# Optimization experiments

Measured on AMD Instinct MI355X. Metric: run time of the kernel, lower is better.

Reference implementation:

```python
import jax, jax.numpy as jnp
import numpy as np

EMBED_DIM = 1024
NUM_HEADS = 16
HEAD_DIM = EMBED_DIM // NUM_HEADS


def setup_inputs() -> dict:
    key = jax.random.key(0)
    ks = jax.random.split(key, 12)
    B, Nq, Nkv, D = 4, 1024, 1024, EMBED_DIM
    s = 1.0 / np.sqrt(D)
    return {
        "query": jax.random.normal(ks[0], (B, Nq, D), jnp.float32),
        "key_value": jax.random.normal(ks[1], (B, Nkv, D), jnp.float32),
        "Wq": jax.random.normal(ks[2], (D, D), jnp.float32) * s,
        "bq": jnp.zeros((D,), jnp.float32),
        "Wk": jax.random.normal(ks[3], (D, D), jnp.float32) * s,
        "bk": jnp.zeros((D,), jnp.float32),
        "Wv": jax.random.normal(ks[4], (D, D), jnp.float32) * s,
        "bv": jnp.zeros((D,), jnp.float32),
        "Wo": jax.random.normal(ks[5], (D, D), jnp.float32) * s,
        "bo": jnp.zeros((D,), jnp.float32),
        "gamma": jnp.ones((D,), jnp.float32),
        "beta": jnp.zeros((D,), jnp.float32),
    }


def reference(query, key_value, Wq, bq, Wk, bk, Wv, bv, Wo, bo, gamma, beta):
    B, Nq, D = query.shape
    Nkv = key_value.shape[1]
    H, Hd = NUM_HEADS, HEAD_DIM
    # projections -> [B, H, N, Hd]
    q = (query @ Wq + bq).reshape(B, Nq, H, Hd).transpose(0, 2, 1, 3)
    k = (key_value @ Wk + bk).reshape(B, Nkv, H, Hd).transpose(0, 2, 1, 3)
    v = (key_value @ Wv + bv).reshape(B, Nkv, H, Hd).transpose(0, 2, 1, 3)
    scores = jnp.einsum("bhqd,bhkd->bhqk", q, k) / jnp.sqrt(jnp.float32(Hd))
    attn = jax.nn.softmax(scores, axis=-1)  # dropout = identity at eval
    out = jnp.einsum("bhqk,bhkd->bhqd", attn, v)
    out = out.transpose(0, 2, 1, 3).reshape(B, Nq, D)
    out = out @ Wo + bo
    # residual + LayerNorm (eps = 1e-5, torch default)
    x = query + out
    mu = jnp.mean(x, axis=-1, keepdims=True)
    var = jnp.mean(jnp.square(x - mu), axis=-1, keepdims=True)
    return (x - mu) / jnp.sqrt(var + 1e-5) * gamma + beta
```

## Files before the change

### kernel.cpp

```cpp
#include <hip/hip_runtime.h>

typedef unsigned short u16;
typedef unsigned int u32;
typedef __attribute__((ext_vector_type(4))) unsigned short u16x4;
typedef __attribute__((ext_vector_type(8))) short short8;
typedef __attribute__((ext_vector_type(4))) float f32x4;

#define MFMA16(a, b, c) __builtin_amdgcn_mfma_f32_16x16x32_bf16(a, b, c, 0, 0, 0)

__device__ __forceinline__ u16 f2bf(float f) {
  unsigned u = __builtin_bit_cast(unsigned, f);
  u += 0x7fffu + ((u >> 16) & 1u);
  return (u16)(u >> 16);
}

__device__ __forceinline__ u32 cvtpk(float lo, float hi) {
  u32 r;
  asm("v_cvt_pk_bf16_f32 %0, %1, %2" : "=v"(r) : "v"(lo), "v"(hi));
  return r;
}

__device__ __forceinline__ float ex2(float x) {
  float r;
  asm("v_exp_f32 %0, %1" : "=v"(r) : "v"(x));
  return r;
}

__device__ __forceinline__ void gl_lds16(const void* g, void* l) {
  __builtin_amdgcn_global_load_lds((const __attribute__((address_space(1))) char*)g,
                                   (__attribute__((address_space(3))) char*)l, 16, 0, 0);
}

__global__ __launch_bounds__(256) void cvt_bf16_k(const float* __restrict__ in,
                                                  u16* __restrict__ out) {
  int i = blockIdx.x * 256 + threadIdx.x;
  float4 v = ((const float4*)in)[i];
  u16x4 o;
  o.x = f2bf(v.x); o.y = f2bf(v.y); o.z = f2bf(v.z); o.w = f2bf(v.w);
  ((u16x4*)out)[i] = o;
}

__global__ __launch_bounds__(256) void wt_k(const float* __restrict__ W0, const float* __restrict__ W1,
                                            const float* __restrict__ W2, const float* __restrict__ W3,
                                            u16* __restrict__ T0, u16* __restrict__ T1,
                                            u16* __restrict__ T2, u16* __restrict__ T3) {
  const float* W; u16* T;
  switch (blockIdx.z) {
    case 0: W = W0; T = T0; break;
    case 1: W = W1; T = T1; break;
    case 2: W = W2; T = T2; break;
    default: W = W3; T = T3; break;
  }
  __shared__ __align__(16) u16 t[64][72];
  const int k0 = blockIdx.y * 64, n0 = blockIdx.x * 64;
  const int tid = threadIdx.x;
  const int r = tid >> 4, c4 = (tid & 15) * 4;
#pragma unroll
  for (int i = 0; i < 4; i++) {
    float4 v = *(const float4*)(W + (k0 + r + i * 16) * 1024 + n0 + c4);
    u16x4 o;
    o.x = f2bf(v.x); o.y = f2bf(v.y); o.z = f2bf(v.z); o.w = f2bf(v.w);
    *(u16x4*)&t[r + i * 16][c4] = o;
  }
  __syncthreads();
#pragma unroll
  for (int i = 0; i < 4; i++) {
    int nr = r + i * 16;
    u16x4 o;
    o.x = t[c4 + 0][nr]; o.y = t[c4 + 1][nr]; o.z = t[c4 + 2][nr]; o.w = t[c4 + 3][nr];
    *(u16x4*)(T + (n0 + nr) * 1024 + k0 + c4) = o;
  }
}

__global__ __launch_bounds__(256, 3) void gemmqkv_k(
    const u16* __restrict__ qbf, const u16* __restrict__ kvbf,
    const u16* __restrict__ Wqt, const u16* __restrict__ Wkt, const u16* __restrict__ Wvt,
    const float* __restrict__ pbq, const float* __restrict__ pbk, const float* __restrict__ pbv,
    u16* __restrict__ Qh, u16* __restrict__ Kh, u16* __restrict__ Vth) {
  const int lin = blockIdx.x;
  const int swz = (lin & 7) * 96 + (lin >> 3);
  const int x = swz & 7, y = (swz >> 3) & 31, z = swz >> 8;

  const u16* A  = (z == 0) ? qbf : kvbf;
  const u16* Bt = (z == 0) ? Wqt : (z == 1 ? Wkt : Wvt);
  const float* bias = (z == 0) ? pbq : (z == 1 ? pbk : pbv);

  __shared__ __align__(16) u16 As[128 * 64];
  __shared__ __align__(16) u16 Bs[128 * 64];
  const int tid = threadIdx.x;
  const int l = tid & 63, w = tid >> 6;
  const int lr = l >> 4, lc = l & 15;
  const int wr = w >> 1, wc = w & 1;
  const int m0 = y * 128, n0 = x * 128;

  f32x4 acc[4][4] = {};

  const int sr = tid >> 2, sc = (tid & 3) * 8;
  const u16* Ag = A + (m0 + sr) * 1024 + sc;
  const u16* Bg = Bt + (n0 + sr) * 1024 + sc;

  for (int k0 = 0; k0 < 1024; k0 += 64) {
    __syncthreads();
    gl_lds16(Ag + k0, As + tid * 8);
    gl_lds16(Ag + 64 * 1024 + k0, As + 2048 + tid * 8);
    gl_lds16(Bg + k0, Bs + tid * 8);
    gl_lds16(Bg + 64 * 1024 + k0, Bs + 2048 + tid * 8);
    gl_lds16(Ag + k0 + 32, As + 4096 + tid * 8);
    gl_lds16(Ag + 64 * 1024 + k0 + 32, As + 6144 + tid * 8);
    gl_lds16(Bg + k0 + 32, Bs + 4096 + tid * 8);
    gl_lds16(Bg + 64 * 1024 + k0 + 32, Bs + 6144 + tid * 8);
    __syncthreads();
    const u16* PA = (z == 2) ? Bs : As;
    const u16* PB = (z == 2) ? As : Bs;
    short8 af[4][2], bf[4][2];
    const int ks8 = lr * 8;
#pragma unroll
    for (int m = 0; m < 4; m++)
#pragma unroll
      for (int h = 0; h < 2; h++)
        af[m][h] = *(const short8*)(PA + h * 4096 + (wr * 64 + m * 16 + lc) * 32 + ks8);
#pragma unroll
    for (int n = 0; n < 4; n++)
#pragma unroll
      for (int h = 0; h < 2; h++)
        bf[n][h] = *(const short8*)(PB + h * 4096 + (wc * 64 + n * 16 + lc) * 32 + ks8);
#pragma unroll
    for (int m = 0; m < 4; m++)
#pragma unroll
      for (int n = 0; n < 4; n++) {
        acc[m][n] = MFMA16(af[m][0], bf[n][0], acc[m][n]);
        acc[m][n] = MFMA16(af[m][1], bf[n][1], acc[m][n]);
      }
  }

  if (z == 2) {
#pragma unroll
    for (int m = 0; m < 4; m++) {
#pragma unroll
      for (int r = 0; r < 4; r++) {
        int ncol = n0 + wr * 64 + m * 16 + lr * 4 + r;
        float bb = bias[ncol];
        int h = ncol >> 6, d = ncol & 63;
#pragma unroll
        for (int n = 0; n < 4; n++) {
          int tok = m0 + wc * 64 + n * 16 + lc;
          Vth[(((tok >> 10) * 16 + h) * 64 + d) * 1024 + (tok & 1023)] =
              f2bf(acc[m][n][r] + bb);
        }
      }
    }
  } else {
    u16* outb = (z == 0) ? Qh : Kh;
    const float scale = (z == 0) ? 0.18033688f : 1.0f;
#pragma unroll
    for (int m = 0; m < 4; m++)
#pragma unroll
      for (int n = 0; n < 4; n++) {
        int ncol = n0 + wc * 64 + n * 16 + lc;
        float bb = bias[ncol];
        int h = ncol >> 6, d = ncol & 63;
#pragma unroll
        for (int r = 0; r < 4; r++) {
          int tok = m0 + wr * 64 + m * 16 + lr * 4 + r;
          outb[(((tok >> 10) * 16 + h) * 1024 + (tok & 1023)) * 64 + d] =
              f2bf((acc[m][n][r] + bb) * scale);
        }
      }
  }
}

__global__ __launch_bounds__(256, 4) void gemmo_k(const u16* __restrict__ A,
                                                  const u16* __restrict__ Bt,
                                                  const float* __restrict__ bias,
                                                  float* __restrict__ outf) {
  const int lin = blockIdx.x;
  const int swz = (lin & 7) * 64 + (lin >> 3);
  const int x = swz & 15, y = swz >> 4;

  __shared__ __align__(16) u16 As[128 * 32];
  __shared__ __align__(16) u16 Bs[64 * 32];
  const int tid = threadIdx.x;
  const int l = tid & 63, w = tid >> 6;
  const int lr = l >> 4, lc = l & 15;
  const int wr = w >> 1, wc = w & 1;
  const int m0 = y * 128, n0 = x * 64;

  f32x4 acc[4][2] = {};
  const int sc = (tid & 3) * 8;
  const u16* Ag = A + (m0 + (tid >> 2)) * 1024 + sc;
  const u16* Bg = Bt + (n0 + (tid >> 2)) * 1024 + sc;

  for (int k0 = 0; k0 < 1024; k0 += 32) {
    __syncthreads();
    gl_lds16(Ag + k0, As + tid * 8);
    gl_lds16(Ag + 64 * 1024 + k0, As + 2048 + tid * 8);
    gl_lds16(Bg + k0, Bs + tid * 8);
    __syncthreads();
    short8 af[4], bf[2];
    const int ks8 = lr * 8;
#pragma unroll
    for (int m = 0; m < 4; m++)
      af[m] = *(const short8*)(As + (wr * 64 + m * 16 + lc) * 32 + ks8);
#pragma unroll
    for (int n = 0; n < 2; n++)
      bf[n] = *(const short8*)(Bs + (wc * 32 + n * 16 + lc) * 32 + ks8);
#pragma unroll
    for (int m = 0; m < 4; m++)
#pragma unroll
      for (int n = 0; n < 2; n++)
        acc[m][n] = MFMA16(af[m], bf[n], acc[m][n]);
  }
#pragma unroll
  for (int m = 0; m < 4; m++)
#pragma unroll
    for (int n = 0; n < 2; n++) {
      int ncol = n0 + wc * 32 + n * 16 + lc;
      float bb = bias[ncol];
#pragma unroll
      for (int r = 0; r < 4; r++) {
        int tok = m0 + wr * 64 + m * 16 + lr * 4 + r;
        outf[tok * 1024 + ncol] = acc[m][n][r] + bb;
      }
    }
}

__global__ __launch_bounds__(256, 4) void attn_k(const u16* __restrict__ Q,
                                                 const u16* __restrict__ K,
                                                 const u16* __restrict__ Vt,
                                                 u16* __restrict__ O) {
  const int bid = blockIdx.x;
  const int xcd = bid & 7, j = bid >> 3;
  const int bh = xcd + 8 * (j & 7);
  const int q0 = (j >> 3) * 64;
  const int tid = threadIdx.x;
  const int w = tid >> 6, l = tid & 63;
  const int lr = l >> 4, lc = l & 15;
  const u16* Qh = Q + bh * (1024 * 64);
  const u16* Kh = K + bh * (1024 * 64);
  const u16* Vh = Vt + bh * (64 * 1024);

  __shared__ __align__(16) u16 Ks[2][64 * 64];
  __shared__ __align__(16) u16 Vs[2][64 * 64];
  __shared__ __align__(16) u32 Plds[4][16][32];

  const int st_row = tid >> 3;
  const int st_cb = (tid & 7) * 16;
  const int sw1 = (st_cb ^ ((st_row & 7) << 4)) >> 1;
  const int st_row2 = st_row + 32;
  const int sw2 = (st_cb ^ ((st_row2 & 7) << 4)) >> 1;

  short8 bq[2];
#pragma unroll
  for (int ks = 0; ks < 2; ks++)
    bq[ks] = *(const short8*)(Qh + (q0 + w * 16 + lc) * 64 + ks * 32 + lr * 8);

  f32x4 oacc[4] = {};
  float mrun = -1e30f, lrun = 0.f;

  gl_lds16(Kh + st_row * 64 + sw1, &Ks[0][tid * 8]);
  gl_lds16(Kh + st_row2 * 64 + sw2, &Ks[0][2048 + tid * 8]);
  gl_lds16(Vh + st_row * 1024 + sw1, &Vs[0][tid * 8]);
  gl_lds16(Vh + st_row2 * 1024 + sw2, &Vs[0][2048 + tid * 8]);

  const int xw = (lc & 7) << 2;

  for (int t = 0; t < 16; ++t) {
    const int pb = t & 1;
    if (t < 15) {
      const int kvn = (t + 1) * 64;
      gl_lds16(Kh + (kvn + st_row) * 64 + sw1, &Ks[pb ^ 1][tid * 8]);
      gl_lds16(Kh + (kvn + st_row2) * 64 + sw2, &Ks[pb ^ 1][2048 + tid * 8]);
      gl_lds16(Vh + st_row * 1024 + kvn + sw1, &Vs[pb ^ 1][tid * 8]);
      gl_lds16(Vh + st_row2 * 1024 + kvn + sw2, &Vs[pb ^ 1][2048 + tid * 8]);
      asm volatile("s_waitcnt vmcnt(4)" ::: "memory");
    } else {
      asm volatile("s_waitcnt vmcnt(0)" ::: "memory");
    }
    __builtin_amdgcn_s_barrier();
    asm volatile("" ::: "memory");

    const u16* Kb = Ks[pb];
    const u16* Vb = Vs[pb];

    f32x4 s[4] = {};
    __builtin_amdgcn_s_setprio(1);
#pragma unroll
    for (int mk = 0; mk < 4; mk++) {
      const int krow = mk * 16 + lc;
      const u16* kp = Kb + krow * 64;
#pragma unroll
      for (int ks = 0; ks < 2; ks++) {
        const int cb = (ks * 64 + lr * 16) ^ ((krow & 7) << 4);
        short8 ak = *(const short8*)(kp + (cb >> 1));
        s[mk] = MFMA16(ak, bq[ks], s[mk]);
      }
    }
    __builtin_amdgcn_s_setprio(0);

    float mx;
    {
      float a = fmaxf(fmaxf(s[0][0], s[0][1]), fmaxf(s[0][2], s[0][3]));
      float b = fmaxf(fmaxf(s[1][0], s[1][1]), fmaxf(s[1][2], s[1][3]));
      float c = fmaxf(fmaxf(s[2][0], s[2][1]), fmaxf(s[2][2], s[2][3]));
      float d = fmaxf(fmaxf(s[3][0], s[3][1]), fmaxf(s[3][2], s[3][3]));
      mx = fmaxf(fmaxf(a, b), fmaxf(c, d));
    }
    mx = fmaxf(mx, __shfl_xor(mx, 16));
    mx = fmaxf(mx, __shfl_xor(mx, 32));

    if (!__all(mx <= mrun + 8.f)) {
      float mnew = fmaxf(mrun, mx);
      float alpha = ex2(mrun - mnew);
      mrun = mnew;
      lrun *= alpha;
      float alr[4];
#pragma unroll
      for (int r = 0; r < 4; r++) alr[r] = __shfl(alpha, lr * 4 + r);
#pragma unroll
      for (int nd = 0; nd < 4; nd++)
#pragma unroll
        for (int r = 0; r < 4; r++) oacc[nd][r] *= alr[r];
    }

#pragma unroll
    for (int mk = 0; mk < 4; mk++)
#pragma unroll
      for (int r = 0; r < 4; r++) s[mk][r] = ex2(s[mk][r] - mrun);
    float ps;
    {
      float a = (s[0][0] + s[0][1]) + (s[0][2] + s[0][3]);
      float b = (s[1][0] + s[1][1]) + (s[1][2] + s[1][3]);
      float c = (s[2][0] + s[2][1]) + (s[2][2] + s[2][3]);
      float d = (s[3][0] + s[3][1]) + (s[3][2] + s[3][3]);
      ps = (a + b) + (c + d);
    }
    ps += __shfl_xor(ps, 16);
    ps += __shfl_xor(ps, 32);
    lrun += ps;

    u32* PW = &Plds[w][lc][0];
#pragma unroll
    for (int mk = 0; mk < 4; mk++)
#pragma unroll
      for (int rr = 0; rr < 2; rr++)
        PW[(mk * 8 + lr * 2 + rr) ^ xw] = cvtpk(s[mk][2 * rr], s[mk][2 * rr + 1]);

    __builtin_amdgcn_s_setprio(1);
#pragma unroll
    for (int ks = 0; ks < 2; ks++) {
      short8 ap = *(const short8*)&Plds[w][lc][(ks * 16 + lr * 4) ^ xw];
#pragma unroll
      for (int nd = 0; nd < 4; nd++) {
        const int vrow = nd * 16 + lc;
        const int cb = (ks * 64 + lr * 16) ^ ((vrow & 7) << 4);
        short8 bv = *(const short8*)(Vb + vrow * 64 + (cb >> 1));
        oacc[nd] = MFMA16(ap, bv, oacc[nd]);
      }
    }
    __builtin_amdgcn_s_setprio(0);

    asm volatile("" ::: "memory");
    __builtin_amdgcn_s_barrier();
  }

  float inv = 1.f / lrun;
  float invr[4];
#pragma unroll
  for (int r = 0; r < 4; r++) invr[r] = __shfl(inv, lr * 4 + r);
  const int b = bh >> 4, h = bh & 15;
#pragma unroll
  for (int r = 0; r < 4; r++) {
    int row = b * 1024 + q0 + w * 16 + lr * 4 + r;
#pragma unroll
    for (int nd = 0; nd < 4; nd++)
      O[row * 1024 + h * 64 + nd * 16 + lc] = f2bf(oacc[nd][r] * invr[r]);
  }
}

__global__ __launch_bounds__(256) void ln_k(const float* __restrict__ q,
                                            const float* __restrict__ p2,
                                            const float* __restrict__ gamma,
                                            const float* __restrict__ beta,
                                            float* __restrict__ out) {
  const int row = blockIdx.x, tid = threadIdx.x;
  float4 xq = ((const float4*)(q + row * 1024))[tid];
  float4 xp = ((const float4*)(p2 + row * 1024))[tid];
  float4 x = {xq.x + xp.x, xq.y + xp.y, xq.z + xp.z, xq.w + xp.w};
  float s = x.x + x.y + x.z + x.w;
#pragma unroll
  for (int off = 1; off < 64; off <<= 1) s += __shfl_xor(s, off);
  __shared__ float red[8];
  const int w = tid >> 6;
  if ((tid & 63) == 0) red[w] = s;
  __syncthreads();
  float mu = (red[0] + red[1] + red[2] + red[3]) * (1.0f / 1024.0f);
  float4 dx = {x.x - mu, x.y - mu, x.z - mu, x.w - mu};
  float s2 = dx.x * dx.x + dx.y * dx.y + dx.z * dx.z + dx.w * dx.w;
#pragma unroll
  for (int off = 1; off < 64; off <<= 1) s2 += __shfl_xor(s2, off);
  if ((tid & 63) == 0) red[4 + w] = s2;
  __syncthreads();
  float var = (red[4] + red[5] + red[6] + red[7]) * (1.0f / 1024.0f);
  float rs = rsqrtf(var + 1e-5f);
  float4 g = ((const float4*)gamma)[tid];
  float4 bb = ((const float4*)beta)[tid];
  float4 o = {dx.x * rs * g.x + bb.x, dx.y * rs * g.y + bb.y,
              dx.z * rs * g.z + bb.z, dx.w * rs * g.w + bb.w};
  ((float4*)(out + row * 1024))[tid] = o;
}

extern "C" void kernel_launch(void* const* d_in, const int* in_sizes, int n_in,
                              void* d_out, int out_size, void* d_ws, size_t ws_size,
                              hipStream_t stream) {
  const float* query = (const float*)d_in[0];
  const float* kv    = (const float*)d_in[1];
  const float* Wq = (const float*)d_in[2];
  const float* bq = (const float*)d_in[3];
  const float* Wk = (const float*)d_in[4];
  const float* bk = (const float*)d_in[5];
  const float* Wv = (const float*)d_in[6];
  const float* bv = (const float*)d_in[7];
  const float* Wo = (const float*)d_in[8];
  const float* bo = (const float*)d_in[9];
  const float* gamma = (const float*)d_in[10];
  const float* beta  = (const float*)d_in[11];
  float* out = (float*)d_out;

  char* ws = (char*)d_ws;
  const size_t MB = 1u << 20;
  u16* qbf  = (u16*)(ws + 0 * MB);
  u16* kvbf = (u16*)(ws + 8 * MB);
  u16* Wqt  = (u16*)(ws + 16 * MB);
  u16* Wkt  = (u16*)(ws + 18 * MB);
  u16* Wvt  = (u16*)(ws + 20 * MB);
  u16* Wot  = (u16*)(ws + 22 * MB);
  u16* Qh   = (u16*)(ws + 24 * MB);
  u16* Kh   = (u16*)(ws + 32 * MB);
  u16* Vth  = (u16*)(ws + 40 * MB);
  u16* attO = (u16*)(ws + 48 * MB);
  float* p2 = (float*)(ws + 56 * MB);

  cvt_bf16_k<<<dim3(4096), dim3(256), 0, stream>>>(query, qbf);
  cvt_bf16_k<<<dim3(4096), dim3(256), 0, stream>>>(kv, kvbf);
  wt_k<<<dim3(16, 16, 4), dim3(256), 0, stream>>>(Wq, Wk, Wv, Wo, Wqt, Wkt, Wvt, Wot);

  gemmqkv_k<<<dim3(768), dim3(256), 0, stream>>>(qbf, kvbf, Wqt, Wkt, Wvt,
                                                 bq, bk, bv, Qh, Kh, Vth);

  attn_k<<<dim3(1024), dim3(256), 0, stream>>>(Qh, Kh, Vth, attO);

  gemmo_k<<<dim3(512), dim3(256), 0, stream>>>(attO, Wot, bo, p2);

  ln_k<<<dim3(4096), dim3(256), 0, stream>>>(query, p2, gamma, beta, out);
}
```

Measured before the change: 113.0 us.

## Double query rows per attention block and merge bf16 conversion launches

Each attention block now covers 128 query rows instead of 64. Every wave handles two 16-row groups that share each K/V tile loaded into LDS, which halves the grid and halves K/V global-to-LDS traffic per query. The two fp32-to-bf16 conversion kernels are also merged into a single launch to save one launch. The cost is more registers per thread, with launch bounds dropped to 2 blocks per SIMD, and fewer blocks to keep the device busy.

```diff
diff --git a/kernel.cpp b/kernel.cpp
--- a/kernel.cpp
+++ b/kernel.cpp
@@ -31,9 +31,13 @@
                                    (__attribute__((address_space(3))) char*)l, 16, 0, 0);
 }
 
-__global__ __launch_bounds__(256) void cvt_bf16_k(const float* __restrict__ in,
-                                                  u16* __restrict__ out) {
-  int i = blockIdx.x * 256 + threadIdx.x;
+__global__ __launch_bounds__(256) void cvt2_k(const float* __restrict__ a,
+                                              const float* __restrict__ b,
+                                              u16* __restrict__ oa, u16* __restrict__ ob) {
+  const int bid = blockIdx.x;
+  const float* in = (bid < 4096) ? a : b;
+  u16* out = (bid < 4096) ? oa : ob;
+  int i = (bid & 4095) * 256 + threadIdx.x;
   float4 v = ((const float4*)in)[i];
   u16x4 o;
   o.x = f2bf(v.x); o.y = f2bf(v.y); o.z = f2bf(v.z); o.w = f2bf(v.w);
@@ -224,14 +228,14 @@
     }
 }
 
-__global__ __launch_bounds__(256, 4) void attn_k(const u16* __restrict__ Q,
+__global__ __launch_bounds__(256, 2) void attn_k(const u16* __restrict__ Q,
                                                  const u16* __restrict__ K,
                                                  const u16* __restrict__ Vt,
                                                  u16* __restrict__ O) {
   const int bid = blockIdx.x;
   const int xcd = bid & 7, j = bid >> 3;
   const int bh = xcd + 8 * (j & 7);
-  const int q0 = (j >> 3) * 64;
+  const int q0 = (j >> 3) * 128;
   const int tid = threadIdx.x;
   const int w = tid >> 6, l = tid & 63;
   const int lr = l >> 4, lc = l & 15;
@@ -241,7 +245,7 @@
 
   __shared__ __align__(16) u16 Ks[2][64 * 64];
   __shared__ __align__(16) u16 Vs[2][64 * 64];
-  __shared__ __align__(16) u32 Plds[4][16][32];
+  __shared__ __align__(16) u32 Plds[4][2][16][32];
 
   const int st_row = tid >> 3;
   const int st_cb = (tid & 7) * 16;
@@ -249,13 +253,15 @@
   const int st_row2 = st_row + 32;
   const int sw2 = (st_cb ^ ((st_row2 & 7) << 4)) >> 1;
 
-  short8 bq[2];
-#pragma unroll
-  for (int ks = 0; ks < 2; ks++)
-    bq[ks] = *(const short8*)(Qh + (q0 + w * 16 + lc) * 64 + ks * 32 + lr * 8);
-
-  f32x4 oacc[4] = {};
-  float mrun = -1e30f, lrun = 0.f;
+  short8 bq[2][2];
+#pragma unroll
+  for (int g = 0; g < 2; g++)
+#pragma unroll
+    for (int ks = 0; ks < 2; ks++)
+      bq[g][ks] = *(const short8*)(Qh + (q0 + w * 32 + g * 16 + lc) * 64 + ks * 32 + lr * 8);
+
+  f32x4 oacc[2][4] = {};
+  float mrun[2] = {-1e30f, -1e30f}, lrun[2] = {0.f, 0.f};
 
   gl_lds16(Kh + st_row * 64 + sw1, &Ks[0][tid * 8]);
   gl_lds16(Kh + st_row2 * 64 + sw2, &Ks[0][2048 + tid * 8]);
@@ -282,7 +288,7 @@
     const u16* Kb = Ks[pb];
     const u16* Vb = Vs[pb];
 
-    f32x4 s[4] = {};
+    f32x4 s0[4] = {}, s1[4] = {};
     __builtin_amdgcn_s_setprio(1);
 #pragma unroll
     for (int mk = 0; mk < 4; mk++) {
@@ -292,69 +298,99 @@
       for (int ks = 0; ks < 2; ks++) {
         const int cb = (ks * 64 + lr * 16) ^ ((krow & 7) << 4);
         short8 ak = *(const short8*)(kp + (cb >> 1));
-        s[mk] = MFMA16(ak, bq[ks], s[mk]);
+        s0[mk] = MFMA16(ak, bq[0][ks], s0[mk]);
+        s1[mk] = MFMA16(ak, bq[1][ks], s1[mk]);
       }
     }
     __builtin_amdgcn_s_setprio(0);
 
-    float mx;
+    float mx0, mx1;
     {
-      float a = fmaxf(fmaxf(s[0][0], s[0][1]), fmaxf(s[0][2], s[0][3]));
-      float b = fmaxf(fmaxf(s[1][0], s[1][1]), fmaxf(s[1][2], s[1][3]));
-      float c = fmaxf(fmaxf(s[2][0], s[2][1]), fmaxf(s[2][2], s[2][3]));
-      float d = fmaxf(fmaxf(s[3][0], s[3][1]), fmaxf(s[3][2], s[3][3]));
-      mx = fmaxf(fmaxf(a, b), fmaxf(c, d));
-    }
-    mx = fmaxf(mx, __shfl_xor(mx, 16));
-    mx = fmaxf(mx, __shfl_xor(mx, 32));
-
-    if (!__all(mx <= mrun + 8.f)) {
-      float mnew = fmaxf(mrun, mx);
-      float alpha = ex2(mrun - mnew);
-      mrun = mnew;
-      lrun *= alpha;
-      float alr[4];
-#pragma unroll
-      for (int r = 0; r < 4; r++) alr[r] = __shfl(alpha, lr * 4 + r);
+      float a = fmaxf(fmaxf(s0[0][0], s0[0][1]), fmaxf(s0[0][2], s0[0][3]));
+      float b = fmaxf(fmaxf(s0[1][0], s0[1][1]), fmaxf(s0[1][2], s0[1][3]));
+      float c = fmaxf(fmaxf(s0[2][0], s0[2][1]), fmaxf(s0[2][2], s0[2][3]));
+      float d = fmaxf(fmaxf(s0[3][0], s0[3][1]), fmaxf(s0[3][2], s0[3][3]));
+      mx0 = fmaxf(fmaxf(a, b), fmaxf(c, d));
+      float e = fmaxf(fmaxf(s1[0][0], s1[0][1]), fmaxf(s1[0][2], s1[0][3]));
+      float f = fmaxf(fmaxf(s1[1][0], s1[1][1]), fmaxf(s1[1][2], s1[1][3]));
+      float g2 = fmaxf(fmaxf(s1[2][0], s1[2][1]), fmaxf(s1[2][2], s1[2][3]));
+      float h = fmaxf(fmaxf(s1[3][0], s1[3][1]), fmaxf(s1[3][2], s1[3][3]));
+      mx1 = fmaxf(fmaxf(e, f), fmaxf(g2, h));
+    }
+    mx0 = fmaxf(mx0, __shfl_xor(mx0, 16));
+    mx0 = fmaxf(mx0, __shfl_xor(mx0, 32));
+    mx1 = fmaxf(mx1, __shfl_xor(mx1, 16));
+    mx1 = fmaxf(mx1, __shfl_xor(mx1, 32));
+
+    if (!__all(mx0 <= mrun[0] + 8.f && mx1 <= mrun[1] + 8.f)) {
+      float mn0 = fmaxf(mrun[0], mx0), mn1 = fmaxf(mrun[1], mx1);
+      float al0 = ex2(mrun[0] - mn0), al1 = ex2(mrun[1] - mn1);
+      mrun[0] = mn0; mrun[1] = mn1;
+      lrun[0] *= al0; lrun[1] *= al1;
+      float a0[4], a1[4];
+#pragma unroll
+      for (int r = 0; r < 4; r++) {
+        a0[r] = __shfl(al0, lr * 4 + r);
+        a1[r] = __shfl(al1, lr * 4 + r);
+      }
 #pragma unroll
       for (int nd = 0; nd < 4; nd++)
 #pragma unroll
-        for (int r = 0; r < 4; r++) oacc[nd][r] *= alr[r];
-    }
-
+        for (int r = 0; r < 4; r++) {
+          oacc[0][nd][r] *= a0[r];
+          oacc[1][nd][r] *= a1[r];
+        }
+    }
+
+    u32* PW0 = &Plds[w][0][lc][0];
+    u32* PW1 = &Plds[w][1][lc][0];
 #pragma unroll
     for (int mk = 0; mk < 4; mk++)
 #pragma unroll
-      for (int r = 0; r < 4; r++) s[mk][r] = ex2(s[mk][r] - mrun);
-    float ps;
+      for (int r = 0; r < 4; r++) {
+        s0[mk][r] = ex2(s0[mk][r] - mrun[0]);
+        s1[mk][r] = ex2(s1[mk][r] - mrun[1]);
+      }
+    float ps0, ps1;
     {
-      float a = (s[0][0] + s[0][1]) + (s[0][2] + s[0][3]);
-      float b = (s[1][0] + s[1][1]) + (s[1][2] + s[1][3]);
-      float c = (s[2][0] + s[2][1]) + (s[2][2] + s[2][3]);
-      float d = (s[3][0] + s[3][1]) + (s[3][2] + s[3][3]);
-      ps = (a + b) + (c + d);
-    }
-    ps += __shfl_xor(ps, 16);
-    ps += __shfl_xor(ps, 32);
-    lrun += ps;
-
-    u32* PW = &Plds[w][lc][0];
+      float a = (s0[0][0] + s0[0][1]) + (s0[0][2] + s0[0][3]);
+      float b = (s0[1][0] + s0[1][1]) + (s0[1][2] + s0[1][3]);
+      float c = (s0[2][0] + s0[2][1]) + (s0[2][2] + s0[2][3]);
+      float d = (s0[3][0] + s0[3][1]) + (s0[3][2] + s0[3][3]);
+      ps0 = (a + b) + (c + d);
+      float e = (s1[0][0] + s1[0][1]) + (s1[0][2] + s1[0][3]);
+      float f = (s1[1][0] + s1[1][1]) + (s1[1][2] + s1[1][3]);
+      float g2 = (s1[2][0] + s1[2][1]) + (s1[2][2] + s1[2][3]);
+      float h = (s1[3][0] + s1[3][1]) + (s1[3][2] + s1[3][3]);
+      ps1 = (e + f) + (g2 + h);
+    }
+    ps0 += __shfl_xor(ps0, 16);
+    ps0 += __shfl_xor(ps0, 32);
+    ps1 += __shfl_xor(ps1, 16);
+    ps1 += __shfl_xor(ps1, 32);
+    lrun[0] += ps0;
+    lrun[1] += ps1;
+
 #pragma unroll
     for (int mk = 0; mk < 4; mk++)
 #pragma unroll
-      for (int rr = 0; rr < 2; rr++)
-        PW[(mk * 8 + lr * 2 + rr) ^ xw] = cvtpk(s[mk][2 * rr], s[mk][2 * rr + 1]);
+      for (int rr = 0; rr < 2; rr++) {
+        PW0[(mk * 8 + lr * 2 + rr) ^ xw] = cvtpk(s0[mk][2 * rr], s0[mk][2 * rr + 1]);
+        PW1[(mk * 8 + lr * 2 + rr) ^ xw] = cvtpk(s1[mk][2 * rr], s1[mk][2 * rr + 1]);
+      }
 
     __builtin_amdgcn_s_setprio(1);
 #pragma unroll
     for (int ks = 0; ks < 2; ks++) {
-      short8 ap = *(const short8*)&Plds[w][lc][(ks * 16 + lr * 4) ^ xw];
+      short8 ap0 = *(const short8*)&Plds[w][0][lc][(ks * 16 + lr * 4) ^ xw];
+      short8 ap1 = *(const short8*)&Plds[w][1][lc][(ks * 16 + lr * 4) ^ xw];
 #pragma unroll
       for (int nd = 0; nd < 4; nd++) {
         const int vrow = nd * 16 + lc;
         const int cb = (ks * 64 + lr * 16) ^ ((vrow & 7) << 4);
         short8 bv = *(const short8*)(Vb + vrow * 64 + (cb >> 1));
-        oacc[nd] = MFMA16(ap, bv, oacc[nd]);
+        oacc[0][nd] = MFMA16(ap0, bv, oacc[0][nd]);
+        oacc[1][nd] = MFMA16(ap1, bv, oacc[1][nd]);
       }
     }
     __builtin_amdgcn_s_setprio(0);
@@ -363,17 +399,20 @@
     __builtin_amdgcn_s_barrier();
   }
 
-  float inv = 1.f / lrun;
-  float invr[4];
-#pragma unroll
-  for (int r = 0; r < 4; r++) invr[r] = __shfl(inv, lr * 4 + r);
   const int b = bh >> 4, h = bh & 15;
 #pragma unroll
-  for (int r = 0; r < 4; r++) {
-    int row = b * 1024 + q0 + w * 16 + lr * 4 + r;
-#pragma unroll
-    for (int nd = 0; nd < 4; nd++)
-      O[row * 1024 + h * 64 + nd * 16 + lc] = f2bf(oacc[nd][r] * invr[r]);
+  for (int g = 0; g < 2; g++) {
+    float inv = 1.f / lrun[g];
+    float invr[4];
+#pragma unroll
+    for (int r = 0; r < 4; r++) invr[r] = __shfl(inv, lr * 4 + r);
+#pragma unroll
+    for (int r = 0; r < 4; r++) {
+      int row = b * 1024 + q0 + w * 32 + g * 16 + lr * 4 + r;
+#pragma unroll
+      for (int nd = 0; nd < 4; nd++)
+        O[row * 1024 + h * 64 + nd * 16 + lc] = f2bf(oacc[g][nd][r] * invr[r]);
+    }
   }
 }
 
@@ -440,14 +479,13 @@
   u16* attO = (u16*)(ws + 48 * MB);
   float* p2 = (float*)(ws + 56 * MB);
 
-  cvt_bf16_k<<<dim3(4096), dim3(256), 0, stream>>>(query, qbf);
-  cvt_bf16_k<<<dim3(4096), dim3(256), 0, stream>>>(kv, kvbf);
+  cvt2_k<<<dim3(8192), dim3(256), 0, stream>>>(query, kv, qbf, kvbf);
   wt_k<<<dim3(16, 16, 4), dim3(256), 0, stream>>>(Wq, Wk, Wv, Wo, Wqt, Wkt, Wvt, Wot);
 
   gemmqkv_k<<<dim3(768), dim3(256), 0, stream>>>(qbf, kvbf, Wqt, Wkt, Wvt,
                                                  bq, bk, bv, Qh, Kh, Vth);
 
-  attn_k<<<dim3(1024), dim3(256), 0, stream>>>(Qh, Kh, Vth, attO);
+  attn_k<<<dim3(512), dim3(256), 0, stream>>>(Qh, Kh, Vth, attO);
 
   gemmo_k<<<dim3(512), dim3(256), 0, stream>>>(attO, Wot, bo, p2);
 
```

After: 108.2 us. 4.3% less time.
